# Kernel tuning notes

Measured on AMD Instinct MI355X. Metric: run time of the kernel, lower is better.

Reference implementation:

```python
import jax, jax.numpy as jnp
import numpy as np

D = 512

def _linear(x, W, b):
    # torch Linear: x @ W.T + b, W is [out, in]
    return jnp.einsum('bnd,od->bno', x, W) + b

def _attend(Q, K, V):
    # scores: [B, N, N]
    s = jnp.einsum('bnd,bmd->bnm', Q, K)
    a = jax.nn.softmax(s, axis=-1)
    # F.normalize(p=1, dim=-1): divide by sum of abs (softmax is nonneg, sums to 1,
    # but stay faithful to the original math)
    a = a / jnp.clip(jnp.sum(jnp.abs(a), axis=-1, keepdims=True), 1e-12)
    a = a / jnp.sqrt(jnp.asarray(D, a.dtype))
    return jnp.einsum('bnm,bmd->bnd', a, V)

def setup_inputs() -> dict:
    key = jax.random.key(0)
    ks = jax.random.split(key, 12)
    B, N = 2, 4096
    lim = 1.0 / np.sqrt(D)
    lim2 = 1.0 / np.sqrt(2 * D)
    return {
        'x_f': jax.random.normal(ks[0], (B, N, D), jnp.float32),
        'x_s': jax.random.normal(ks[1], (B, N, D), jnp.float32),
        'Wq': jax.random.uniform(ks[2], (D, D), jnp.float32, -lim, lim),
        'bq': jax.random.uniform(ks[3], (D,), jnp.float32, -lim, lim),
        'Wk': jax.random.uniform(ks[4], (D, D), jnp.float32, -lim, lim),
        'bk': jax.random.uniform(ks[5], (D,), jnp.float32, -lim, lim),
        'Wv': jax.random.uniform(ks[6], (D, D), jnp.float32, -lim, lim),
        'bv': jax.random.uniform(ks[7], (D,), jnp.float32, -lim, lim),
        'Wc': jax.random.uniform(ks[8], (D, 2 * D), jnp.float32, -lim2, lim2),
        'bc': jax.random.uniform(ks[9], (D,), jnp.float32, -lim2, lim2),
    }

def reference(x_f, x_s, Wq, bq, Wk, bk, Wv, bv, Wc, bc):
    # dropout layers are identity in eval mode
    co_occur = jax.nn.relu(_linear(jnp.concatenate([x_f, x_s], axis=-1), Wc, bc))
    # f -> s direction
    out_f = _attend(_linear(x_f, Wq, bq), _linear(x_s, Wk, bk), _linear(x_f, Wv, bv)) + co_occur
    # s -> f direction
    out_s = _attend(_linear(x_s, Wq, bq), _linear(x_f, Wk, bk), _linear(x_s, Wv, bv)) + co_occur
    return (out_f, out_s)
```

## Files before the change

kernel.cpp:

```cpp
#include <hip/hip_runtime.h>
#include <stdint.h>


using bf16x8 = __attribute__((ext_vector_type(8))) short;
using f32x4  = __attribute__((ext_vector_type(4))) float;

typedef __attribute__((address_space(1))) const void as1_void_t;
typedef __attribute__((address_space(3))) void as3_void_t;

__device__ __forceinline__ void gload16(const void* g, void* l) {
  __builtin_amdgcn_global_load_lds((as1_void_t*)g, (as3_void_t*)l, 16, 0, 0);
}

__device__ __forceinline__ unsigned f2bf_u(float f) {
  unsigned u = __float_as_uint(f);
  return (u + 0x7fffu + ((u >> 16) & 1u)) >> 16;
}

#define MFMA_BF16(a, b, c) __builtin_amdgcn_mfma_f32_16x16x32_bf16((a), (b), (c), 0, 0, 0)

__global__ void cvt_bf16(const float* __restrict__ src,
                         unsigned short* __restrict__ dst, int n4) {
  int i = blockIdx.x * blockDim.x + threadIdx.x;
  if (i >= n4) return;
  float4 v = ((const float4*)src)[i];
  uint2 o;
  o.x = f2bf_u(v.x) | (f2bf_u(v.y) << 16);
  o.y = f2bf_u(v.z) | (f2bf_u(v.w) << 16);
  ((uint2*)dst)[i] = o;
}

__global__ void split_wc(const float* __restrict__ Wc,
                         unsigned short* __restrict__ Wf,
                         unsigned short* __restrict__ Ws) {
  int t = blockIdx.x * blockDim.x + threadIdx.x;
  int row = t >> 7, col = (t & 127) * 4;
  float4 a = *(const float4*)(Wc + row * 1024 + col);
  float4 b = *(const float4*)(Wc + row * 1024 + 512 + col);
  uint2 oa, ob;
  oa.x = f2bf_u(a.x) | (f2bf_u(a.y) << 16);
  oa.y = f2bf_u(a.z) | (f2bf_u(a.w) << 16);
  ob.x = f2bf_u(b.x) | (f2bf_u(b.y) << 16);
  ob.y = f2bf_u(b.z) | (f2bf_u(b.w) << 16);
  *(uint2*)(Wf + row * 512 + col) = oa;
  *(uint2*)(Ws + row * 512 + col) = ob;
}

template<int EPI>
__global__ void __launch_bounds__(256)
gemm_proj(const unsigned short* __restrict__ A1,
          const unsigned short* __restrict__ A2,
          const unsigned short* __restrict__ W1,
          const unsigned short* __restrict__ W2,
          const float* __restrict__ bias,
          void* __restrict__ Cout, int nk) {
  __shared__ __align__(16) unsigned short As[128 * 32];
  __shared__ __align__(16) unsigned short Bs[128 * 32];
  const int tid = threadIdx.x;
  const int w = tid >> 6, lane = tid & 63;
  const int m0 = blockIdx.x * 128, n0 = blockIdx.y * 128;
  const int wm = (w >> 1) * 64, wn = (w & 1) * 64;
  f32x4 acc[4][4] = {};

  for (int ks = 0; ks < nk; ++ks) {
    const unsigned short* Ab = (EPI == 2 && ks >= 16) ? A2 : A1;
    const unsigned short* Wb = (EPI == 2 && ks >= 16) ? W2 : W1;
    const int k0 = (EPI == 2) ? ((ks & 15) * 32) : (ks * 32);
#pragma unroll
    for (int t = 0; t < 2; ++t) {
      const int o = t * 256 + tid;
      const int row = o >> 2, seg = o & 3;
      gload16(Ab + (size_t)(m0 + row) * 512 + k0 + seg * 8,
              (char*)As + t * 4096 + w * 1024);
      gload16(Wb + (size_t)(n0 + row) * 512 + k0 + seg * 8,
              (char*)Bs + t * 4096 + w * 1024);
    }
    __syncthreads();
    bf16x8 a[4], b[4];
#pragma unroll
    for (int i = 0; i < 4; ++i) {
      a[i] = *(const bf16x8*)(As + (wm + i * 16 + (lane & 15)) * 32 + (lane >> 4) * 8);
      b[i] = *(const bf16x8*)(Bs + (wn + i * 16 + (lane & 15)) * 32 + (lane >> 4) * 8);
    }
#pragma unroll
    for (int i = 0; i < 4; ++i)
#pragma unroll
      for (int j = 0; j < 4; ++j)
        acc[i][j] = MFMA_BF16(a[i], b[j], acc[i][j]);
    __syncthreads();
  }

  const int lm = lane >> 4, ln = lane & 15;
  if (EPI == 0) {
    unsigned short* Cb = (unsigned short*)Cout;
#pragma unroll
    for (int i = 0; i < 4; ++i)
#pragma unroll
      for (int j = 0; j < 4; ++j) {
        const int col = n0 + wn + j * 16 + ln;
        const float bv = bias[col];
#pragma unroll
        for (int r = 0; r < 4; ++r) {
          const int row = m0 + wm + i * 16 + lm * 4 + r;
          Cb[(size_t)row * 512 + col] = (unsigned short)f2bf_u(acc[i][j][r] + bv);
        }
      }
  } else if (EPI == 1) {
    unsigned short* Cb = (unsigned short*)Cout;
#pragma unroll
    for (int i = 0; i < 4; ++i)
#pragma unroll
      for (int j = 0; j < 4; ++j) {
        const int col = n0 + wn + j * 16 + ln;
        const float bv = bias[col];
#pragma unroll
        for (int r = 0; r < 4; ++r) {
          const int row = m0 + wm + i * 16 + lm * 4 + r;
          const int sb = row >> 12, n = row & 4095;
          Cb[(size_t)(sb * 512 + col) * 4096 + n] = (unsigned short)f2bf_u(acc[i][j][r] + bv);
        }
      }
  } else {
    float* Cb = (float*)Cout;
#pragma unroll
    for (int i = 0; i < 4; ++i)
#pragma unroll
      for (int j = 0; j < 4; ++j) {
        const int col = n0 + wn + j * 16 + ln;
        const float bv = bias[col];
#pragma unroll
        for (int r = 0; r < 4; ++r) {
          const int row = m0 + wm + i * 16 + lm * 4 + r;
          float v = acc[i][j][r] + bv;
          Cb[(size_t)row * 512 + col] = v > 0.f ? v : 0.f;
        }
      }
  }
}

__global__ void __launch_bounds__(512)
flash_attn(const unsigned short* __restrict__ Qb,
           const unsigned short* __restrict__ Kb,
           const unsigned short* __restrict__ Vt,
           const float* __restrict__ CO,
           float* __restrict__ Out) {
  __shared__ __align__(16) unsigned short Ks[32 * 512];
  __shared__ __align__(16) unsigned short Vs[512 * 32];
  __shared__ __align__(16) float S_lds[64 * 33];
  __shared__ __align__(16) unsigned short P_lds[64 * 48];
  __shared__ float m_run[64], l_run[64], alpha_l[64];

  const int tid = threadIdx.x;
  const int w = tid >> 6, lane = tid & 63;
  const int q0 = blockIdx.x * 64;
  const int b = blockIdx.y, dir = blockIdx.z;
  const int qw = w >> 1, kw = w & 1;

  const size_t qbase  = (size_t)(dir * 2 + b) * 4096 * 512;
  const size_t kbase  = (size_t)((1 - dir) * 2 + b) * 4096 * 512;
  const size_t vbase  = (size_t)(dir * 2 + b) * 512 * 4096;
  const size_t cobase = (size_t)b * 4096 * 512;
  const size_t obase  = qbase;

  if (tid < 64) { m_run[tid] = -1e30f; l_run[tid] = 0.0f; }

  bf16x8 qf[16];
  {
    const int qrow = q0 + qw * 16 + (lane & 15);
#pragma unroll
    for (int g = 0; g < 16; ++g)
      qf[g] = *(const bf16x8*)(Qb + qbase + (size_t)qrow * 512 + g * 32 + (lane >> 4) * 8);
  }

  f32x4 o_acc[4][4] = {};
  __syncthreads();

  for (int kt = 0; kt < 128; ++kt) {
    const int kv0 = kt * 32;
#pragma unroll
    for (int t = 0; t < 4; ++t) {
      const int krow = t * 8 + w;
      gload16(Kb + kbase + (size_t)(kv0 + krow) * 512 + (lane ^ (krow & 7)) * 8,
              (char*)Ks + krow * 1024);
      const int dbase = (t * 8 + w) * 16;
      const int d = dbase + (lane >> 2);
      gload16(Vt + vbase + (size_t)d * 4096 + kv0 + (((lane & 3) ^ (d & 3)) * 8),
              (char*)Vs + dbase * 64);
    }
    __syncthreads();

    f32x4 s = {};
    {
      const int krow = kw * 16 + (lane & 15);
#pragma unroll
      for (int g = 0; g < 16; ++g) {
        const int chunk = (g * 4 + (lane >> 4)) ^ (krow & 7);
        bf16x8 kf = *(const bf16x8*)((const char*)Ks + krow * 1024 + chunk * 16);
        s = MFMA_BF16(qf[g], kf, s);
      }
      const int col = kw * 16 + (lane & 15);
      const int rb = qw * 16 + (lane >> 4) * 4;
#pragma unroll
      for (int r = 0; r < 4; ++r)
        S_lds[(rb + r) * 33 + col] = s[r];
    }
    __syncthreads();

    {
      const int row = w * 8 + (lane >> 3);
      const int j = lane & 7;
      const float* Sr = &S_lds[row * 33 + j * 4];
      float v0 = Sr[0], v1 = Sr[1], v2 = Sr[2], v3 = Sr[3];
      float mx = fmaxf(fmaxf(v0, v1), fmaxf(v2, v3));
      mx = fmaxf(mx, __shfl_xor(mx, 1));
      mx = fmaxf(mx, __shfl_xor(mx, 2));
      mx = fmaxf(mx, __shfl_xor(mx, 4));
      const float mold = m_run[row];
      const float mnew = fmaxf(mold, mx);
      float p0 = __expf(v0 - mnew), p1 = __expf(v1 - mnew);
      float p2 = __expf(v2 - mnew), p3 = __expf(v3 - mnew);
      float ls = p0 + p1 + p2 + p3;
      ls += __shfl_xor(ls, 1);
      ls += __shfl_xor(ls, 2);
      ls += __shfl_xor(ls, 4);
      const float alpha = __expf(mold - mnew);
      if (j == 0) {
        m_run[row] = mnew;
        l_run[row] = l_run[row] * alpha + ls;
        alpha_l[row] = alpha;
      }
      uint2 pw;
      pw.x = f2bf_u(p0) | (f2bf_u(p1) << 16);
      pw.y = f2bf_u(p2) | (f2bf_u(p3) << 16);
      *(uint2*)(P_lds + row * 48 + j * 4) = pw;
    }
    __syncthreads();

#pragma unroll
    for (int qi = 0; qi < 4; ++qi) {
      bf16x8 pa = *(const bf16x8*)(P_lds + (qi * 16 + (lane & 15)) * 48 + (lane >> 4) * 8);
#pragma unroll
      for (int r = 0; r < 4; ++r) {
        const float al = alpha_l[qi * 16 + (lane >> 4) * 4 + r];
#pragma unroll
        for (int di = 0; di < 4; ++di)
          o_acc[qi][di][r] *= al;
      }
#pragma unroll
      for (int di = 0; di < 4; ++di) {
        const int d = w * 64 + di * 16 + (lane & 15);
        const int slot = (lane >> 4) ^ (d & 3);
        bf16x8 vf = *(const bf16x8*)((const char*)Vs + d * 64 + slot * 16);
        o_acc[qi][di] = MFMA_BF16(pa, vf, o_acc[qi][di]);
      }
    }
    __syncthreads();
  }

  const float rsd = 0.04419417382415922f;
#pragma unroll
  for (int qi = 0; qi < 4; ++qi) {
#pragma unroll
    for (int r = 0; r < 4; ++r) {
      const int ql = qi * 16 + (lane >> 4) * 4 + r;
      const float inv = rsd / l_run[ql];
      const size_t rowoff = (size_t)(q0 + ql) * 512;
#pragma unroll
      for (int di = 0; di < 4; ++di) {
        const int d = w * 64 + di * 16 + (lane & 15);
        Out[obase + rowoff + d] = o_acc[qi][di][r] * inv + CO[cobase + rowoff + d];
      }
    }
  }
}

extern "C" void kernel_launch(void* const* d_in, const int* in_sizes, int n_in,
                              void* d_out, int out_size, void* d_ws, size_t ws_size,
                              hipStream_t stream) {
  const float* x_f = (const float*)d_in[0];
  const float* x_s = (const float*)d_in[1];
  const float* Wq  = (const float*)d_in[2];
  const float* bq  = (const float*)d_in[3];
  const float* Wk  = (const float*)d_in[4];
  const float* bk  = (const float*)d_in[5];
  const float* Wv  = (const float*)d_in[6];
  const float* bv  = (const float*)d_in[7];
  const float* Wc  = (const float*)d_in[8];
  const float* bc  = (const float*)d_in[9];
  float* out = (float*)d_out;

  unsigned short* Xb  = (unsigned short*)d_ws;
  unsigned short* Qb  = Xb + 8388608;
  unsigned short* Kb  = Qb + 8388608;
  unsigned short* Vt  = Kb + 8388608;
  float*          CO  = (float*)(Vt + 8388608);
  unsigned short* Wqb = (unsigned short*)(CO + 4194304);
  unsigned short* Wkb = Wqb + 262144;
  unsigned short* Wvb = Wkb + 262144;
  unsigned short* Wcf = Wvb + 262144;
  unsigned short* Wcs = Wcf + 262144;

  cvt_bf16<<<4096, 256, 0, stream>>>(x_f, Xb, 1048576);
  cvt_bf16<<<4096, 256, 0, stream>>>(x_s, Xb + 4194304, 1048576);
  cvt_bf16<<<256, 256, 0, stream>>>(Wq, Wqb, 65536);
  cvt_bf16<<<256, 256, 0, stream>>>(Wk, Wkb, 65536);
  cvt_bf16<<<256, 256, 0, stream>>>(Wv, Wvb, 65536);
  split_wc<<<256, 256, 0, stream>>>(Wc, Wcf, Wcs);

  dim3 gQ(128, 4);
  gemm_proj<0><<<gQ, 256, 0, stream>>>(Xb, nullptr, Wqb, nullptr, bq, Qb, 16);
  gemm_proj<0><<<gQ, 256, 0, stream>>>(Xb, nullptr, Wkb, nullptr, bk, Kb, 16);
  gemm_proj<1><<<gQ, 256, 0, stream>>>(Xb, nullptr, Wvb, nullptr, bv, Vt, 16);
  dim3 gC(64, 4);
  gemm_proj<2><<<gC, 256, 0, stream>>>(Xb, Xb + 4194304, Wcf, Wcs, bc, CO, 32);

  dim3 gF(64, 2, 2);
  flash_attn<<<gF, 512, 0, stream>>>(Qb, Kb, Vt, CO, out);
}
```

Measured before the change: 504.3 us.

## Double-buffer LDS tiles in projection GEMM and flash attention with prefetch

Both the projection GEMM and the flash-attention kernel now keep two LDS buffers and issue async global-to-LDS loads for the next K/V (or A/W) tile before computing on the current one. The aim is to hide global memory latency behind MFMA work. __syncthreads calls are replaced by explicit waitcnt plus s_barrier macros, and the trailing barrier per iteration is dropped. The QK^T reduction is split into two independent accumulator chains, and S_lds padding and alpha loads are vectorized. LDS use roughly doubles, which may reduce occupancy, and the more aggressive barrier scheme carries some risk of ordering hazards.

```diff
diff --git a/kernel.cpp b/kernel.cpp
--- a/kernel.cpp
+++ b/kernel.cpp
@@ -11,6 +11,20 @@
 __device__ __forceinline__ void gload16(const void* g, void* l) {
   __builtin_amdgcn_global_load_lds((as1_void_t*)g, (as3_void_t*)l, 16, 0, 0);
 }
+
+#define BAR_VM0()                                                  \
+  do {                                                             \
+    asm volatile("s_waitcnt vmcnt(0) lgkmcnt(0)" ::: "memory");    \
+    __builtin_amdgcn_s_barrier();                                  \
+    __builtin_amdgcn_sched_barrier(0);                             \
+  } while (0)
+
+#define BAR_LGKM()                                                 \
+  do {                                                             \
+    asm volatile("s_waitcnt lgkmcnt(0)" ::: "memory");             \
+    __builtin_amdgcn_s_barrier();                                  \
+    __builtin_amdgcn_sched_barrier(0);                             \
+  } while (0)
 
 __device__ __forceinline__ unsigned f2bf_u(float f) {
   unsigned u = __float_as_uint(f);
@@ -54,15 +68,15 @@
           const unsigned short* __restrict__ W2,
           const float* __restrict__ bias,
           void* __restrict__ Cout, int nk) {
-  __shared__ __align__(16) unsigned short As[128 * 32];
-  __shared__ __align__(16) unsigned short Bs[128 * 32];
+  __shared__ __align__(16) unsigned short As[2][128 * 32];
+  __shared__ __align__(16) unsigned short Bs[2][128 * 32];
   const int tid = threadIdx.x;
   const int w = tid >> 6, lane = tid & 63;
   const int m0 = blockIdx.x * 128, n0 = blockIdx.y * 128;
   const int wm = (w >> 1) * 64, wn = (w & 1) * 64;
   f32x4 acc[4][4] = {};
 
-  for (int ks = 0; ks < nk; ++ks) {
+  auto stage = [&](int ks, int bi) {
     const unsigned short* Ab = (EPI == 2 && ks >= 16) ? A2 : A1;
     const unsigned short* Wb = (EPI == 2 && ks >= 16) ? W2 : W1;
     const int k0 = (EPI == 2) ? ((ks & 15) * 32) : (ks * 32);
@@ -71,23 +85,28 @@
       const int o = t * 256 + tid;
       const int row = o >> 2, seg = o & 3;
       gload16(Ab + (size_t)(m0 + row) * 512 + k0 + seg * 8,
-              (char*)As + t * 4096 + w * 1024);
+              (char*)As[bi] + t * 4096 + w * 1024);
       gload16(Wb + (size_t)(n0 + row) * 512 + k0 + seg * 8,
-              (char*)Bs + t * 4096 + w * 1024);
-    }
-    __syncthreads();
+              (char*)Bs[bi] + t * 4096 + w * 1024);
+    }
+  };
+
+  stage(0, 0);
+  for (int ks = 0; ks < nk; ++ks) {
+    const int bi = ks & 1;
+    BAR_VM0();
+    if (ks + 1 < nk) stage(ks + 1, bi ^ 1);
     bf16x8 a[4], b[4];
 #pragma unroll
     for (int i = 0; i < 4; ++i) {
-      a[i] = *(const bf16x8*)(As + (wm + i * 16 + (lane & 15)) * 32 + (lane >> 4) * 8);
-      b[i] = *(const bf16x8*)(Bs + (wn + i * 16 + (lane & 15)) * 32 + (lane >> 4) * 8);
+      a[i] = *(const bf16x8*)(As[bi] + (wm + i * 16 + (lane & 15)) * 32 + (lane >> 4) * 8);
+      b[i] = *(const bf16x8*)(Bs[bi] + (wn + i * 16 + (lane & 15)) * 32 + (lane >> 4) * 8);
     }
 #pragma unroll
     for (int i = 0; i < 4; ++i)
 #pragma unroll
       for (int j = 0; j < 4; ++j)
         acc[i][j] = MFMA_BF16(a[i], b[j], acc[i][j]);
-    __syncthreads();
   }
 
   const int lm = lane >> 4, ln = lane & 15;
@@ -144,11 +163,13 @@
            const unsigned short* __restrict__ Vt,
            const float* __restrict__ CO,
            float* __restrict__ Out) {
-  __shared__ __align__(16) unsigned short Ks[32 * 512];
-  __shared__ __align__(16) unsigned short Vs[512 * 32];
-  __shared__ __align__(16) float S_lds[64 * 33];
+  __shared__ __align__(16) unsigned short Ks[2][32 * 512];
+  __shared__ __align__(16) unsigned short Vs[2][512 * 32];
+  __shared__ __align__(16) float S_lds[64 * 36];
   __shared__ __align__(16) unsigned short P_lds[64 * 48];
-  __shared__ float m_run[64], l_run[64], alpha_l[64];
+  __shared__ __align__(16) float m_run[64];
+  __shared__ __align__(16) float l_run[64];
+  __shared__ __align__(16) float alpha_l[64];
 
   const int tid = threadIdx.x;
   const int w = tid >> 6, lane = tid & 63;
@@ -162,7 +183,23 @@
   const size_t cobase = (size_t)b * 4096 * 512;
   const size_t obase  = qbase;
 
+  auto stage_tiles = [&](int kt, int bi) {
+    const int kv0 = kt * 32;
+#pragma unroll
+    for (int t = 0; t < 4; ++t) {
+      const int krow = t * 8 + w;
+      gload16(Kb + kbase + (size_t)(kv0 + krow) * 512 + (lane ^ (krow & 7)) * 8,
+              (char*)Ks[bi] + krow * 1024);
+      const int dbase = (t * 8 + w) * 16;
+      const int d = dbase + (lane >> 2);
+      gload16(Vt + vbase + (size_t)d * 4096 + kv0 + (((lane & 3) ^ (d & 3)) * 8),
+              (char*)Vs[bi] + dbase * 64);
+    }
+  };
+
   if (tid < 64) { m_run[tid] = -1e30f; l_run[tid] = 0.0f; }
+
+  stage_tiles(0, 0);
 
   bf16x8 qf[16];
   {
@@ -173,52 +210,47 @@
   }
 
   f32x4 o_acc[4][4] = {};
-  __syncthreads();
 
   for (int kt = 0; kt < 128; ++kt) {
-    const int kv0 = kt * 32;
-#pragma unroll
-    for (int t = 0; t < 4; ++t) {
-      const int krow = t * 8 + w;
-      gload16(Kb + kbase + (size_t)(kv0 + krow) * 512 + (lane ^ (krow & 7)) * 8,
-              (char*)Ks + krow * 1024);
-      const int dbase = (t * 8 + w) * 16;
-      const int d = dbase + (lane >> 2);
-      gload16(Vt + vbase + (size_t)d * 4096 + kv0 + (((lane & 3) ^ (d & 3)) * 8),
-              (char*)Vs + dbase * 64);
-    }
-    __syncthreads();
-
-    f32x4 s = {};
+    const int bi = kt & 1;
+    const unsigned short* Kc = Ks[bi];
+    const unsigned short* Vc = Vs[bi];
+
+    BAR_VM0();
+    if (kt < 127) stage_tiles(kt + 1, bi ^ 1);
+
     {
       const int krow = kw * 16 + (lane & 15);
-#pragma unroll
-      for (int g = 0; g < 16; ++g) {
-        const int chunk = (g * 4 + (lane >> 4)) ^ (krow & 7);
-        bf16x8 kf = *(const bf16x8*)((const char*)Ks + krow * 1024 + chunk * 16);
-        s = MFMA_BF16(qf[g], kf, s);
+      f32x4 s0 = {}, s1 = {};
+#pragma unroll
+      for (int g = 0; g < 8; ++g) {
+        const int c0 = (g * 4 + (lane >> 4)) ^ (krow & 7);
+        const int c1 = ((g + 8) * 4 + (lane >> 4)) ^ (krow & 7);
+        bf16x8 k0 = *(const bf16x8*)((const char*)Kc + krow * 1024 + c0 * 16);
+        bf16x8 k1 = *(const bf16x8*)((const char*)Kc + krow * 1024 + c1 * 16);
+        s0 = MFMA_BF16(qf[g], k0, s0);
+        s1 = MFMA_BF16(qf[g + 8], k1, s1);
       }
       const int col = kw * 16 + (lane & 15);
       const int rb = qw * 16 + (lane >> 4) * 4;
 #pragma unroll
       for (int r = 0; r < 4; ++r)
-        S_lds[(rb + r) * 33 + col] = s[r];
-    }
-    __syncthreads();
+        S_lds[(rb + r) * 36 + col] = s0[r] + s1[r];
+    }
+    BAR_LGKM();
 
     {
       const int row = w * 8 + (lane >> 3);
       const int j = lane & 7;
-      const float* Sr = &S_lds[row * 33 + j * 4];
-      float v0 = Sr[0], v1 = Sr[1], v2 = Sr[2], v3 = Sr[3];
-      float mx = fmaxf(fmaxf(v0, v1), fmaxf(v2, v3));
+      f32x4 sv = *(const f32x4*)&S_lds[row * 36 + j * 4];
+      float mx = fmaxf(fmaxf(sv[0], sv[1]), fmaxf(sv[2], sv[3]));
       mx = fmaxf(mx, __shfl_xor(mx, 1));
       mx = fmaxf(mx, __shfl_xor(mx, 2));
       mx = fmaxf(mx, __shfl_xor(mx, 4));
       const float mold = m_run[row];
       const float mnew = fmaxf(mold, mx);
-      float p0 = __expf(v0 - mnew), p1 = __expf(v1 - mnew);
-      float p2 = __expf(v2 - mnew), p3 = __expf(v3 - mnew);
+      float p0 = __expf(sv[0] - mnew), p1 = __expf(sv[1] - mnew);
+      float p2 = __expf(sv[2] - mnew), p3 = __expf(sv[3] - mnew);
       float ls = p0 + p1 + p2 + p3;
       ls += __shfl_xor(ls, 1);
       ls += __shfl_xor(ls, 2);
@@ -234,28 +266,26 @@
       pw.y = f2bf_u(p2) | (f2bf_u(p3) << 16);
       *(uint2*)(P_lds + row * 48 + j * 4) = pw;
     }
-    __syncthreads();
+    BAR_LGKM();
 
 #pragma unroll
     for (int qi = 0; qi < 4; ++qi) {
       bf16x8 pa = *(const bf16x8*)(P_lds + (qi * 16 + (lane & 15)) * 48 + (lane >> 4) * 8);
-#pragma unroll
-      for (int r = 0; r < 4; ++r) {
-        const float al = alpha_l[qi * 16 + (lane >> 4) * 4 + r];
-#pragma unroll
-        for (int di = 0; di < 4; ++di)
-          o_acc[qi][di][r] *= al;
-      }
+      f32x4 al4 = *(const f32x4*)&alpha_l[qi * 16 + (lane >> 4) * 4];
+#pragma unroll
+      for (int di = 0; di < 4; ++di)
+        o_acc[qi][di] *= al4;
 #pragma unroll
       for (int di = 0; di < 4; ++di) {
         const int d = w * 64 + di * 16 + (lane & 15);
         const int slot = (lane >> 4) ^ (d & 3);
-        bf16x8 vf = *(const bf16x8*)((const char*)Vs + d * 64 + slot * 16);
+        bf16x8 vf = *(const bf16x8*)((const char*)Vc + d * 64 + slot * 16);
         o_acc[qi][di] = MFMA_BF16(pa, vf, o_acc[qi][di]);
       }
     }
-    __syncthreads();
-  }
+  }
+
+  BAR_LGKM();
 
   const float rsd = 0.04419417382415922f;
 #pragma unroll
```

Result: faster. 490.2 us (-2.8%).
